# Performance work log

Measured on AMD Instinct MI355X. Metric: run time of the kernel, lower is better.

Reference implementation:

```python
import jax, jax.numpy as jnp
import numpy as np

H, D = 12, 128          # heads, head_dim
DIM = 1536              # vid_dim == txt_dim == H*D
EPS = 1e-6


def _rmsnorm(x, w):
    # RMSNorm over last dim (head_dim) with learnable scale
    var = jnp.mean(jnp.square(x), axis=-1, keepdims=True)
    return x * jax.lax.rsqrt(var + EPS) * w


def setup_inputs() -> dict:
    key = jax.random.key(0)
    ks = jax.random.split(key, 16)
    B, Lv, Lt = 2, 2 * 24 * 40, 128
    inner = H * D
    s = 0.02
    inp = {
        "vid": jax.random.normal(ks[0], (B * Lv, DIM), jnp.float32),
        "txt": jax.random.normal(ks[1], (B * Lt, DIM), jnp.float32),
        "Wqkv_vid": jax.random.normal(ks[2], (DIM, 3 * inner), jnp.float32) * s,
        "bqkv_vid": jnp.zeros((3 * inner,), jnp.float32),
        "Wqkv_txt": jax.random.normal(ks[3], (DIM, 3 * inner), jnp.float32) * s,
        "bqkv_txt": jnp.zeros((3 * inner,), jnp.float32),
        "nq_vid": jnp.ones((D,), jnp.float32),
        "nk_vid": jnp.ones((D,), jnp.float32),
        "nq_txt": jnp.ones((D,), jnp.float32),
        "nk_txt": jnp.ones((D,), jnp.float32),
        "Wout_vid": jax.random.normal(ks[4], (inner, DIM), jnp.float32) * s,
        "bout_vid": jnp.zeros((DIM,), jnp.float32),
        "Wout_txt": jax.random.normal(ks[5], (inner, DIM), jnp.float32) * s,
        "bout_txt": jnp.zeros((DIM,), jnp.float32),
        # static per-sample shapes (numpy => usable as Python ints under jit)
        "vid_shape": np.array([[2, 24, 40], [2, 24, 40]], np.int64),
        "txt_shape": np.array([[128], [128]], np.int64),
    }
    return inp


def reference(vid, txt, Wqkv_vid, bqkv_vid, Wqkv_txt, bqkv_txt,
              nq_vid, nk_vid, nq_txt, nk_txt,
              Wout_vid, bout_vid, Wout_txt, bout_txt,
              vid_shape, txt_shape):
    B = vid_shape.shape[0]
    Lv = int(np.prod(vid_shape[0]))   # equal lengths across batch
    Lt = int(txt_shape[0, 0])

    # fused QKV projections (separate weights for vid/txt, shared_weights=False)
    vid_qkv = (vid @ Wqkv_vid + bqkv_vid).reshape(-1, 3, H, D)
    txt_qkv = (txt @ Wqkv_txt + bqkv_txt).reshape(-1, 3, H, D)
    vq, vk, vv = vid_qkv[:, 0], vid_qkv[:, 1], vid_qkv[:, 2]
    tq, tk, tv = txt_qkv[:, 0], txt_qkv[:, 1], txt_qkv[:, 2]

    # QK-norm (per-modality RMSNorm over head_dim)
    vq, tq = _rmsnorm(vq, nq_vid), _rmsnorm(tq, nq_txt)
    vk, tk = _rmsnorm(vk, nk_vid), _rmsnorm(tk, nk_txt)

    # multimodal packing: per sample, vid tokens then txt tokens (cu_seqlens over vid_len+txt_len)
    def pack(v, t):
        v = v.reshape(B, Lv, H, D)
        t = t.reshape(B, Lt, H, D)
        return jnp.concatenate([v, t], axis=1)  # [B, Lv+Lt, H, D]

    q = pack(vq, tq).astype(jnp.bfloat16)
    k = pack(vk, tk).astype(jnp.bfloat16)
    v = pack(vv, tv).astype(jnp.bfloat16)

    scale = 1.0 / np.sqrt(D)
    scores = jnp.einsum('blhd,bmhd->bhlm', q, k,
                        preferred_element_type=jnp.float32) * scale
    probs = jax.nn.softmax(scores, axis=-1)
    out = jnp.einsum('bhlm,bmhd->blhd', probs.astype(jnp.bfloat16), v,
                     preferred_element_type=jnp.float32).astype(vid.dtype)

    # unconcat + head merge
    out = out.reshape(B, Lv + Lt, H * D)
    vid_out = out[:, :Lv].reshape(B * Lv, H * D)
    txt_out = out[:, Lv:].reshape(B * Lt, H * D)

    vid_out = vid_out @ Wout_vid + bout_vid
    txt_out = txt_out @ Wout_txt + bout_txt
    return (vid_out, txt_out)
```

## Files before the change

kernel.cpp:

```cpp
#include <hip/hip_runtime.h>
#include <hip/hip_bf16.h>
#include <stdint.h>

typedef __attribute__((ext_vector_type(8))) short  short8;
typedef __attribute__((ext_vector_type(4))) float  f32x4;
typedef __attribute__((ext_vector_type(4))) unsigned int uint4v;
typedef __attribute__((ext_vector_type(4))) unsigned short ushort4v;

#define MFMA16(a,b,c) __builtin_amdgcn_mfma_f32_16x16x32_bf16((a),(b),(c),0,0,0)

#define AS1 __attribute__((address_space(1)))
#define AS3 __attribute__((address_space(3)))
static __device__ __forceinline__ void gload16(void* lds, const void* g) {
  __builtin_amdgcn_global_load_lds((AS1 const void*)g, (AS3 void*)lds, 16, 0, 0);
}

static __device__ __forceinline__ unsigned short f2bf(float x) {
  unsigned int u = __float_as_uint(x);
  u += 0x7fffu + ((u >> 16) & 1u);
  return (unsigned short)(u >> 16);
}
static __device__ __forceinline__ float bf2f(unsigned short h) {
  return __uint_as_float(((unsigned int)h) << 16);
}

#define HDS   12
#define DD    128
#define DIMK  1536
#define NIN   4608
#define LV    1920
#define LT    128
#define LL    2048
#define BB    2
#define MV    3840
#define MT    256
#define MTOT  4096
#define QSC   (0.08838834764831845f * 1.4426950408889634f)

__global__ __launch_bounds__(256) void split_x(const float* __restrict__ vid,
                                               const float* __restrict__ txt,
                                               unsigned short* __restrict__ xhi) {
  size_t i = ((size_t)blockIdx.x * 256 + threadIdx.x) * 4;
  const size_t NV = (size_t)MV * DIMK;
  const float* src = (i < NV) ? (vid + i) : (txt + (i - NV));
  f32x4 v = *(const f32x4*)src;
  ushort4v hv;
#pragma unroll
  for (int j = 0; j < 4; ++j) hv[j] = f2bf(v[j]);
  *(ushort4v*)(xhi + i) = hv;
}

__global__ __launch_bounds__(256) void transpose_cast(const float* __restrict__ W,
                                                      unsigned short* __restrict__ Thi,
                                                      int K, int N) {
  __shared__ float tile[32][33];
  const int tx = threadIdx.x & 31, ty = threadIdx.x >> 5;
  const int k0 = blockIdx.y * 32, n0 = blockIdx.x * 32;
#pragma unroll
  for (int i = 0; i < 32; i += 8)
    tile[ty + i][tx] = W[(size_t)(k0 + ty + i) * N + n0 + tx];
  __syncthreads();
#pragma unroll
  for (int i = 0; i < 32; i += 8)
    Thi[(size_t)(n0 + ty + i) * K + k0 + tx] = f2bf(tile[tx][ty + i]);
}

__global__ __launch_bounds__(256) void vt_transpose(const unsigned short* __restrict__ v,
                                                    unsigned short* __restrict__ vtb) {
  __shared__ unsigned short tile[32][33];
  const int tx = threadIdx.x & 31, ty = threadIdx.x >> 5;
  const int bh = blockIdx.z;
  const int l0 = blockIdx.x * 32, d0 = blockIdx.y * 32;
  const size_t base = (size_t)bh * LL * DD;
#pragma unroll
  for (int i = 0; i < 32; i += 8)
    tile[ty + i][tx] = v[base + (size_t)(l0 + ty + i) * DD + d0 + tx];
  __syncthreads();
#pragma unroll
  for (int i = 0; i < 32; i += 8)
    vtb[base + (size_t)(d0 + ty + i) * LL + l0 + tx] = tile[tx][ty + i];
}

__device__ __forceinline__ void bf16_mainloop256(
    const unsigned short* __restrict__ Ahi, const unsigned short* __restrict__ Bhi,
    int m0, int n0,
    uint4v* __restrict__ sA, uint4v* __restrict__ sB,
    f32x4 (&acc)[4][4]) {
  const int t = threadIdx.x;
  const int lane = t & 63;
  const int w = t >> 6;
  const int wm = w >> 1, wn = w & 1;
  const int lr = lane & 15, lg = lane >> 4;
  const int ra = t >> 1, ca = (t & 1) * 2;
  const int rb = t >> 2, cb = t & 3;
  const size_t arow = (size_t)(m0 + ra) * DIMK + ca * 8;
  const size_t brow = (size_t)(n0 + rb) * DIMK + cb * 8;
  const int sa0 = ca * 256 + ra, sa1 = (ca + 1) * 256 + ra;
  const int sb0 = cb * 128 + rb;
  const int fA = lg * 256 + wm * 64 + lr;
  const int fB = lg * 128 + wn * 64 + lr;

  uint4v va0 = *(const uint4v*)(Ahi + arow);
  uint4v va1 = *(const uint4v*)(Ahi + arow + 8);
  uint4v vb0 = *(const uint4v*)(Bhi + brow);

  int cur = 0;
  for (int k0 = 0; k0 < DIMK; k0 += 32) {
    const int ha = cur * 1024, hb = cur * 512;
    sA[ha + sa0] = va0; sA[ha + sa1] = va1;
    sB[hb + sb0] = vb0;
    if (k0 + 32 < DIMK) {
      va0 = *(const uint4v*)(Ahi + arow + k0 + 32);
      va1 = *(const uint4v*)(Ahi + arow + k0 + 40);
      vb0 = *(const uint4v*)(Bhi + brow + k0 + 32);
    }
    __syncthreads();
    short8 ah[4], bh[4];
#pragma unroll
    for (int i = 0; i < 4; ++i) {
      ah[i] = *(const short8*)&sA[ha + fA + i * 16];
      bh[i] = *(const short8*)&sB[hb + fB + i * 16];
    }
#pragma unroll
    for (int mi = 0; mi < 4; ++mi)
#pragma unroll
      for (int ni = 0; ni < 4; ++ni)
        acc[mi][ni] = MFMA16(ah[mi], bh[ni], acc[mi][ni]);
    cur ^= 1;
  }
}

__global__ __launch_bounds__(512) void gemm_qkv(
    const unsigned short* __restrict__ Xhi,
    const unsigned short* __restrict__ WvH, const unsigned short* __restrict__ WtH,
    const float* __restrict__ bias_v, const float* __restrict__ bias_t,
    const float* __restrict__ nq_v, const float* __restrict__ nk_v,
    const float* __restrict__ nq_t, const float* __restrict__ nk_t,
    unsigned short* __restrict__ qb, unsigned short* __restrict__ kb,
    unsigned short* __restrict__ vb) {
  __shared__ uint4v sA[2048], sB[1024];
  __shared__ float rowsq[2][256];
  const int t = threadIdx.x;
  const int lane = t & 63;
  const int w = t >> 6;
  const int wm = w >> 1, wn = w & 1;
  const int lr = lane & 15, lg = lane >> 4;
  const int bid = blockIdx.x;
  const int xcd = bid & 7, ii = bid >> 3;
  const int mt = xcd * 2 + (ii & 1), nt = ii >> 1;
  const int m0 = mt * 256, n0 = nt * 128;
  const bool istxt = (m0 >= MV);
  const unsigned short* WThi = istxt ? WtH : WvH;
  const float* bias = istxt ? bias_t : bias_v;
  const int Lmod = istxt ? LT : LV;
  const int loff = istxt ? LV : 0;
  const int mbase = istxt ? MV : 0;

  f32x4 acc[4][4];
#pragma unroll
  for (int mi = 0; mi < 4; ++mi)
#pragma unroll
    for (int ni = 0; ni < 4; ++ni) acc[mi][ni] = (f32x4){0.f, 0.f, 0.f, 0.f};

  bf16_mainloop256(Xhi, WThi, m0, n0, sA, sB, acc);

  const int s  = n0 / DIMK;
  const int hh = (n0 % DIMK) / DD;
#pragma unroll
  for (int ni = 0; ni < 4; ++ni) {
    float bv = bias[n0 + wn * 64 + ni * 16 + lr];
#pragma unroll
    for (int mi = 0; mi < 4; ++mi)
#pragma unroll
      for (int r = 0; r < 4; ++r) acc[mi][ni][r] += bv;
  }
  if (s < 2) {
    __syncthreads();
#pragma unroll
    for (int mi = 0; mi < 4; ++mi)
#pragma unroll
      for (int r = 0; r < 4; ++r) {
        float p = 0.f;
#pragma unroll
        for (int ni = 0; ni < 4; ++ni) p += acc[mi][ni][r] * acc[mi][ni][r];
        p += __shfl_xor(p, 1); p += __shfl_xor(p, 2);
        p += __shfl_xor(p, 4); p += __shfl_xor(p, 8);
        if (lr == 0) rowsq[wn][wm * 64 + mi * 16 + lg * 4 + r] = p;
      }
    __syncthreads();
    const float* nw = (s == 0) ? (istxt ? nq_t : nq_v) : (istxt ? nk_t : nk_v);
    const float post = (s == 0) ? QSC : 1.0f;
    float nwv[4];
#pragma unroll
    for (int ni = 0; ni < 4; ++ni) nwv[ni] = nw[wn * 64 + ni * 16 + lr] * post;
#pragma unroll
    for (int mi = 0; mi < 4; ++mi)
#pragma unroll
      for (int r = 0; r < 4; ++r) {
        int row = wm * 64 + mi * 16 + lg * 4 + r;
        float a = (rowsq[0][row] + rowsq[1][row]) * (1.f / 128.f) + 1e-6f;
        float x = rsqrtf(a);
        x = x * (1.5f - 0.5f * a * x * x);
#pragma unroll
        for (int ni = 0; ni < 4; ++ni) acc[mi][ni][r] *= x * nwv[ni];
      }
  }
  unsigned short* dst = (s == 0) ? qb : ((s == 1) ? kb : vb);
#pragma unroll
  for (int mi = 0; mi < 4; ++mi)
#pragma unroll
    for (int r = 0; r < 4; ++r) {
      int mrow = m0 + wm * 64 + mi * 16 + lg * 4 + r - mbase;
      int bidx = (mrow >= Lmod) ? 1 : 0;
      int l = loff + mrow - bidx * Lmod;
      size_t rb2 = ((size_t)(bidx * HDS + hh) * LL + l) * DD;
#pragma unroll
      for (int ni = 0; ni < 4; ++ni) {
        int d = wn * 64 + ni * 16 + lr;
        dst[rb2 + d] = f2bf(acc[mi][ni][r]);
      }
    }
}

__global__ __launch_bounds__(256) void attn_kernel(
    const unsigned short* __restrict__ qb, const unsigned short* __restrict__ kb,
    const unsigned short* __restrict__ vt,
    unsigned short* __restrict__ aohi) {
  const int t = threadIdx.x;
  const int lane = t & 63, w = t >> 6;
  const int lr = lane & 15, lg = lane >> 4;
  const int bid = blockIdx.x;
  const int xcd = bid & 7, ii = bid >> 3;
  const int bh = xcd * 3 + (ii >> 5);
  const int qt = ii & 31;
  const int q0 = (qt * 4 + w) * 16;
  const size_t base = (size_t)bh * LL * DD;

  __shared__ __align__(16) unsigned short Kbuf[2][32 * 128];
  __shared__ __align__(16) unsigned short Vbuf[2][128 * 32];
  __shared__ __align__(16) unsigned short P[4][16 * 40];

  const char* kglob = (const char*)(kb + base);
  const char* vglob = (const char*)(vt + base);

  const int  srcK  = (t * 16) ^ (((t >> 4) & 7) << 4);
  const size_t vs0 = (size_t)(t >> 2) * (LL * 2) +
                     (((t & 3) ^ ((t >> 2) & 3)) << 4);
  const size_t vs1 = vs0 + (size_t)64 * (LL * 2);
  char* kd0 = (char*)Kbuf + w * 1024;
  char* kd1 = kd0 + 4096;
  char* vd0 = (char*)Vbuf + w * 1024;
  char* vd1 = vd0 + 4096;

  int akr[2][4];
#pragma unroll
  for (int h = 0; h < 2; ++h) {
    const int rr = 2 * lr + h;
#pragma unroll
    for (int ks = 0; ks < 4; ++ks)
      akr[h][ks] = rr * 256 + ((ks * 64 + lg * 16) ^ ((rr & 7) << 4));
  }
  const int av0 = lr * 64 + ((lg ^ (lr & 3)) << 4);
  char* pwr = (char*)P + w * 1280 + lg * 320 + lr * 4;
  const char* prd = (const char*)P + w * 1280 + lr * 80 + lg * 16;
  const char* KB = (const char*)Kbuf;
  const char* VB = (const char*)Vbuf;

  short8 qf[4];
#pragma unroll
  for (int ks = 0; ks < 4; ++ks)
    qf[ks] = *(const short8*)(qb + base + (size_t)(q0 + lr) * DD + ks * 32 + lg * 8);

  f32x4 o[8];
#pragma unroll
  for (int i = 0; i < 8; ++i) o[i] = (f32x4){0.f, 0.f, 0.f, 0.f};
  float Z[4] = {0.f, 0.f, 0.f, 0.f};

  const char* gkp = kglob;
  const char* gvp = vglob;
  gload16(kd0, gkp + srcK);
  gload16(kd1, gkp + 4096 + srcK);
  gload16(vd0, gvp + vs0);
  gload16(vd1, gvp + vs1);
  __syncthreads();

#pragma unroll 2
  for (int kt = 0; kt < LL / 32; ++kt) {
    const int cur = kt & 1;
    const int cb = cur * 8192, nb = (cur ^ 1) * 8192;
    if (kt + 1 < LL / 32) {
      gload16(kd0 + nb, gkp + 8192 + srcK);
      gload16(kd1 + nb, gkp + 8192 + 4096 + srcK);
      gload16(vd0 + nb, gvp + 64 + vs0);
      gload16(vd1 + nb, gvp + 64 + vs1);
    }
    f32x4 s0a = (f32x4){0.f, 0.f, 0.f, 0.f}, s0b = (f32x4){0.f, 0.f, 0.f, 0.f};
    f32x4 s1a = (f32x4){0.f, 0.f, 0.f, 0.f}, s1b = (f32x4){0.f, 0.f, 0.f, 0.f};
#pragma unroll
    for (int ks = 0; ks < 4; ++ks) {
      short8 k0f = *(const short8*)(KB + cb + akr[0][ks]);
      short8 k1f = *(const short8*)(KB + cb + akr[1][ks]);
      if (ks < 2) { s0a = MFMA16(qf[ks], k0f, s0a); s1a = MFMA16(qf[ks], k1f, s1a); }
      else        { s0b = MFMA16(qf[ks], k0f, s0b); s1b = MFMA16(qf[ks], k1f, s1b); }
    }
#pragma unroll
    for (int r = 0; r < 4; ++r) {
      float p0, p1;
      float sa = s0a[r] + s0b[r];
      float sb = s1a[r] + s1b[r];
      asm("v_exp_f32 %0, %1" : "=v"(p0) : "v"(sa));
      asm("v_exp_f32 %0, %1" : "=v"(p1) : "v"(sb));
      Z[r] += p0 + p1;
      unsigned int u;
      asm("v_cvt_pk_bf16_f32 %0, %1, %2" : "=v"(u) : "v"(p0), "v"(p1));
      *(unsigned int*)(pwr + r * 80) = u;
    }
    short8 pa = *(const short8*)prd;
#pragma unroll
    for (int df = 0; df < 8; ++df) {
      short8 vf = *(const short8*)(VB + cb + df * 1024 + av0);
      o[df] = MFMA16(pa, vf, o[df]);
    }
    __syncthreads();
    gkp += 8192; gvp += 64;
  }

  float invZ[4];
#pragma unroll
  for (int r = 0; r < 4; ++r) {
    Z[r] += __shfl_xor(Z[r], 1); Z[r] += __shfl_xor(Z[r], 2);
    Z[r] += __shfl_xor(Z[r], 4); Z[r] += __shfl_xor(Z[r], 8);
    invZ[r] = 1.0f / Z[r];
  }

  const int b = bh / HDS, h = bh % HDS;
#pragma unroll
  for (int df = 0; df < 8; ++df)
#pragma unroll
    for (int r = 0; r < 4; ++r) {
      int l = q0 + lg * 4 + r;
      size_t row = (l < LV) ? ((size_t)b * LV + l) : ((size_t)MV + b * LT + (l - LV));
      int col = h * DD + df * 16 + lr;
      aohi[row * DIMK + col] = f2bf(o[df][r] * invZ[r]);
    }
}

__device__ __forceinline__ void bf16_mainloop128(
    const unsigned short* __restrict__ Ahi, const unsigned short* __restrict__ Bhi,
    int m0, int n0,
    uint4v* __restrict__ sA, uint4v* __restrict__ sB,
    f32x4 (&acc)[4][4]) {
  const int t = threadIdx.x;
  const int lane = t & 63;
  const int w = t >> 6;
  const int wm = w >> 1, wn = w & 1;
  const int lr = lane & 15, lg = lane >> 4;
  const int sr = t >> 1;
  const int sc = (t & 1) * 2;
  const size_t arow = (size_t)(m0 + sr) * DIMK + sc * 8;
  const size_t brow = (size_t)(n0 + sr) * DIMK + sc * 8;
  const int slot0 = sc * 128 + sr, slot1 = (sc + 1) * 128 + sr;
  const int fA = lg * 128 + wm * 64 + lr;
  const int fB = lg * 128 + wn * 64 + lr;

  uint4v va0 = *(const uint4v*)(Ahi + arow);
  uint4v va1 = *(const uint4v*)(Ahi + arow + 8);
  uint4v vb0 = *(const uint4v*)(Bhi + brow);
  uint4v vb1 = *(const uint4v*)(Bhi + brow + 8);

  int cur = 0;
  for (int k0 = 0; k0 < DIMK; k0 += 32) {
    const int hs = cur * 512;
    sA[hs + slot0] = va0; sA[hs + slot1] = va1;
    sB[hs + slot0] = vb0; sB[hs + slot1] = vb1;
    if (k0 + 32 < DIMK) {
      va0 = *(const uint4v*)(Ahi + arow + k0 + 32);
      va1 = *(const uint4v*)(Ahi + arow + k0 + 40);
      vb0 = *(const uint4v*)(Bhi + brow + k0 + 32);
      vb1 = *(const uint4v*)(Bhi + brow + k0 + 40);
    }
    __syncthreads();
    short8 ah[4], bh[4];
#pragma unroll
    for (int i = 0; i < 4; ++i) {
      ah[i] = *(const short8*)&sA[hs + fA + i * 16];
      bh[i] = *(const short8*)&sB[hs + fB + i * 16];
    }
#pragma unroll
    for (int mi = 0; mi < 4; ++mi)
#pragma unroll
      for (int ni = 0; ni < 4; ++ni)
        acc[mi][ni] = MFMA16(ah[mi], bh[ni], acc[mi][ni]);
    cur ^= 1;
  }
}

__global__ __launch_bounds__(256) void gemm_out(
    const unsigned short* __restrict__ Ahi,
    const unsigned short* __restrict__ WvH, const unsigned short* __restrict__ WtH,
    const float* __restrict__ bias_v, const float* __restrict__ bias_t,
    float* __restrict__ out) {
  __shared__ uint4v sA[1024], sB[1024];
  const int t = threadIdx.x;
  const int lane = t & 63;
  const int w = t >> 6;
  const int wm = w >> 1, wn = w & 1;
  const int lr = lane & 15, lg = lane >> 4;
  const int bid = blockIdx.x;
  const int xcd = bid & 7, ii = bid >> 3;
  const int mt = xcd * 4 + (ii & 3), nt = ii >> 2;
  const int m0 = mt * 128, n0 = nt * 128;
  const bool istxt = (m0 >= MV);
  const unsigned short* WThi = istxt ? WtH : WvH;
  const float* bias = istxt ? bias_t : bias_v;

  f32x4 acc[4][4];
#pragma unroll
  for (int mi = 0; mi < 4; ++mi)
#pragma unroll
    for (int ni = 0; ni < 4; ++ni) acc[mi][ni] = (f32x4){0.f, 0.f, 0.f, 0.f};

  bf16_mainloop128(Ahi, WThi, m0, n0, sA, sB, acc);

#pragma unroll
  for (int ni = 0; ni < 4; ++ni) {
    float bv = bias[n0 + wn * 64 + ni * 16 + lr];
#pragma unroll
    for (int mi = 0; mi < 4; ++mi)
#pragma unroll
      for (int r = 0; r < 4; ++r) {
        size_t row = (size_t)(m0 + wm * 64 + mi * 16 + lg * 4 + r);
        out[row * DIMK + n0 + wn * 64 + ni * 16 + lr] = acc[mi][ni][r] + bv;
      }
  }
}

extern "C" void kernel_launch(void* const* d_in, const int* in_sizes, int n_in,
                              void* d_out, int out_size, void* d_ws, size_t ws_size,
                              hipStream_t stream) {
  (void)in_sizes; (void)n_in; (void)out_size; (void)ws_size;
  const float* vid      = (const float*)d_in[0];
  const float* txt      = (const float*)d_in[1];
  const float* Wqkv_vid = (const float*)d_in[2];
  const float* bqkv_vid = (const float*)d_in[3];
  const float* Wqkv_txt = (const float*)d_in[4];
  const float* bqkv_txt = (const float*)d_in[5];
  const float* nq_vid   = (const float*)d_in[6];
  const float* nk_vid   = (const float*)d_in[7];
  const float* nq_txt   = (const float*)d_in[8];
  const float* nk_txt   = (const float*)d_in[9];
  const float* Wout_vid = (const float*)d_in[10];
  const float* bout_vid = (const float*)d_in[11];
  const float* Wout_txt = (const float*)d_in[12];
  const float* bout_txt = (const float*)d_in[13];
  float* out = (float*)d_out;

  char* ws = (char*)d_ws;
  size_t off = 0;
  auto alloc = [&](size_t bytes) { char* p = ws + off; off += (bytes + 255) & ~(size_t)255; return p; };

  const size_t SZ_X    = (size_t)MTOT * DIMK * 2;
  const size_t SZ_WQKV = (size_t)NIN * DIMK * 2;
  const size_t SZ_WOUT = (size_t)DIMK * DIMK * 2;
  const size_t SZ_QKVB = (size_t)BB * HDS * LL * DD * 2;

  unsigned short* Xhi   = (unsigned short*)alloc(SZ_X);
  unsigned short* WTqvH = (unsigned short*)alloc(SZ_WQKV);
  unsigned short* WTqtH = (unsigned short*)alloc(SZ_WQKV);
  unsigned short* WTovH = (unsigned short*)alloc(SZ_WOUT);
  unsigned short* WTotH = (unsigned short*)alloc(SZ_WOUT);
  unsigned short* QB    = (unsigned short*)alloc(SZ_QKVB);
  unsigned short* KB    = (unsigned short*)alloc(SZ_QKVB);
  unsigned short* VB    = (unsigned short*)alloc(SZ_QKVB);
  unsigned short* VT    = WTqvH;
  unsigned short* AOhi  = Xhi;

  split_x<<<dim3((MTOT * DIMK) / (256 * 4)), dim3(256), 0, stream>>>(vid, txt, Xhi);
  transpose_cast<<<dim3(NIN / 32, DIMK / 32), dim3(256), 0, stream>>>(Wqkv_vid, WTqvH, DIMK, NIN);
  transpose_cast<<<dim3(NIN / 32, DIMK / 32), dim3(256), 0, stream>>>(Wqkv_txt, WTqtH, DIMK, NIN);
  transpose_cast<<<dim3(DIMK / 32, DIMK / 32), dim3(256), 0, stream>>>(Wout_vid, WTovH, DIMK, DIMK);
  transpose_cast<<<dim3(DIMK / 32, DIMK / 32), dim3(256), 0, stream>>>(Wout_txt, WTotH, DIMK, DIMK);
  gemm_qkv<<<dim3(576), dim3(512), 0, stream>>>(
      Xhi, WTqvH, WTqtH, bqkv_vid, bqkv_txt,
      nq_vid, nk_vid, nq_txt, nk_txt, QB, KB, VB);
  vt_transpose<<<dim3(LL / 32, DD / 32, BB * HDS), dim3(256), 0, stream>>>(VB, VT);
  attn_kernel<<<dim3(768), dim3(256), 0, stream>>>(QB, KB, VT, AOhi);
  gemm_out<<<dim3(384), dim3(256), 0, stream>>>(
      AOhi, WTovH, WTotH, bout_vid, bout_txt, out);
}
```

Before: 230.3 us.

## Use 8-wave attention blocks sharing K/V tiles and raise MFMA priority

The attention kernel now runs 512-thread blocks with 8 waves of 16 query rows each, halving the grid to 384 blocks. Each K/V tile loaded into LDS is shared by twice as many query rows, so every thread issues one async load per tile instead of two. s_setprio is raised around the MFMA sections so matrix work is favoured over other waves. The cost is fewer, larger blocks: with 384 blocks on a 256-CU part the work may split unevenly across CUs, and barriers now synchronise 8 waves.

After: 232.1 us. No clear change (+0.8%).

```diff
diff --git a/kernel.cpp b/kernel.cpp
--- a/kernel.cpp
+++ b/kernel.cpp
@@ -222,7 +222,7 @@
     }
 }
 
-__global__ __launch_bounds__(256) void attn_kernel(
+__global__ __launch_bounds__(512) void attn_kernel(
     const unsigned short* __restrict__ qb, const unsigned short* __restrict__ kb,
     const unsigned short* __restrict__ vt,
     unsigned short* __restrict__ aohi) {
@@ -231,14 +231,14 @@
   const int lr = lane & 15, lg = lane >> 4;
   const int bid = blockIdx.x;
   const int xcd = bid & 7, ii = bid >> 3;
-  const int bh = xcd * 3 + (ii >> 5);
-  const int qt = ii & 31;
-  const int q0 = (qt * 4 + w) * 16;
+  const int bh = xcd * 3 + (ii >> 4);
+  const int qt = ii & 15;
+  const int q0 = (qt * 8 + w) * 16;
   const size_t base = (size_t)bh * LL * DD;
 
   __shared__ __align__(16) unsigned short Kbuf[2][32 * 128];
   __shared__ __align__(16) unsigned short Vbuf[2][128 * 32];
-  __shared__ __align__(16) unsigned short P[4][16 * 40];
+  __shared__ __align__(16) unsigned short P[8][16 * 40];
 
   const char* kglob = (const char*)(kb + base);
   const char* vglob = (const char*)(vt + base);
@@ -246,11 +246,8 @@
   const int  srcK  = (t * 16) ^ (((t >> 4) & 7) << 4);
   const size_t vs0 = (size_t)(t >> 2) * (LL * 2) +
                      (((t & 3) ^ ((t >> 2) & 3)) << 4);
-  const size_t vs1 = vs0 + (size_t)64 * (LL * 2);
-  char* kd0 = (char*)Kbuf + w * 1024;
-  char* kd1 = kd0 + 4096;
-  char* vd0 = (char*)Vbuf + w * 1024;
-  char* vd1 = vd0 + 4096;
+  char* kd = (char*)Kbuf + w * 1024;
+  char* vd = (char*)Vbuf + w * 1024;
 
   int akr[2][4];
 #pragma unroll
@@ -263,8 +260,8 @@
   const int av0 = lr * 64 + ((lg ^ (lr & 3)) << 4);
   char* pwr = (char*)P + w * 1280 + lg * 320 + lr * 4;
   const char* prd = (const char*)P + w * 1280 + lr * 80 + lg * 16;
-  const char* KB = (const char*)Kbuf;
-  const char* VB = (const char*)Vbuf;
+  const char* KBp = (const char*)Kbuf;
+  const char* VBp = (const char*)Vbuf;
 
   short8 qf[4];
 #pragma unroll
@@ -278,10 +275,8 @@
 
   const char* gkp = kglob;
   const char* gvp = vglob;
-  gload16(kd0, gkp + srcK);
-  gload16(kd1, gkp + 4096 + srcK);
-  gload16(vd0, gvp + vs0);
-  gload16(vd1, gvp + vs1);
+  gload16(kd, gkp + srcK);
+  gload16(vd, gvp + vs0);
   __syncthreads();
 
 #pragma unroll 2
@@ -289,20 +284,20 @@
     const int cur = kt & 1;
     const int cb = cur * 8192, nb = (cur ^ 1) * 8192;
     if (kt + 1 < LL / 32) {
-      gload16(kd0 + nb, gkp + 8192 + srcK);
-      gload16(kd1 + nb, gkp + 8192 + 4096 + srcK);
-      gload16(vd0 + nb, gvp + 64 + vs0);
-      gload16(vd1 + nb, gvp + 64 + vs1);
+      gload16(kd + nb, gkp + 8192 + srcK);
+      gload16(vd + nb, gvp + 64 + vs0);
     }
     f32x4 s0a = (f32x4){0.f, 0.f, 0.f, 0.f}, s0b = (f32x4){0.f, 0.f, 0.f, 0.f};
     f32x4 s1a = (f32x4){0.f, 0.f, 0.f, 0.f}, s1b = (f32x4){0.f, 0.f, 0.f, 0.f};
+    __builtin_amdgcn_s_setprio(1);
 #pragma unroll
     for (int ks = 0; ks < 4; ++ks) {
-      short8 k0f = *(const short8*)(KB + cb + akr[0][ks]);
-      short8 k1f = *(const short8*)(KB + cb + akr[1][ks]);
+      short8 k0f = *(const short8*)(KBp + cb + akr[0][ks]);
+      short8 k1f = *(const short8*)(KBp + cb + akr[1][ks]);
       if (ks < 2) { s0a = MFMA16(qf[ks], k0f, s0a); s1a = MFMA16(qf[ks], k1f, s1a); }
       else        { s0b = MFMA16(qf[ks], k0f, s0b); s1b = MFMA16(qf[ks], k1f, s1b); }
     }
+    __builtin_amdgcn_s_setprio(0);
 #pragma unroll
     for (int r = 0; r < 4; ++r) {
       float p0, p1;
@@ -316,11 +311,13 @@
       *(unsigned int*)(pwr + r * 80) = u;
     }
     short8 pa = *(const short8*)prd;
+    __builtin_amdgcn_s_setprio(1);
 #pragma unroll
     for (int df = 0; df < 8; ++df) {
-      short8 vf = *(const short8*)(VB + cb + df * 1024 + av0);
+      short8 vf = *(const short8*)(VBp + cb + df * 1024 + av0);
       o[df] = MFMA16(pa, vf, o[df]);
     }
+    __builtin_amdgcn_s_setprio(0);
     __syncthreads();
     gkp += 8192; gvp += 64;
   }
@@ -484,7 +481,7 @@
       Xhi, WTqvH, WTqtH, bqkv_vid, bqkv_txt,
       nq_vid, nk_vid, nq_txt, nk_txt, QB, KB, VB);
   vt_transpose<<<dim3(LL / 32, DD / 32, BB * HDS), dim3(256), 0, stream>>>(VB, VT);
-  attn_kernel<<<dim3(768), dim3(256), 0, stream>>>(QB, KB, VT, AOhi);
+  attn_kernel<<<dim3(384), dim3(512), 0, stream>>>(QB, KB, VT, AOhi);
   gemm_out<<<dim3(384), dim3(256), 0, stream>>>(
       AOhi, WTovH, WTotH, bout_vid, bout_txt, out);
 }
```
